# Kernel optimization log

Hardware: AMD Instinct MI355X
Metric: run time of the kernel (lower is better)

The kernel has to match this reference:

```python
import jax, jax.numpy as jnp
import numpy as np

N_PATCHES = 14
HIDDEN_D = 768
N_HEADS = 12
D_HEAD = HIDDEN_D // N_HEADS
SEQ = N_PATCHES ** 2 + 1  # 197
INPUT_D = 3 * 16 * 16  # c * patch_h * patch_w = 768
LN_EPS = 1e-5


def positional_embeddings(seq_len, d):
    # result[i, j] = sin(i / 10000**(j/d)) if j even else cos(i / 10000**((j-1)/d))
    i = jnp.arange(seq_len, dtype=jnp.float32)[:, None]
    j = jnp.arange(d, dtype=jnp.float32)[None, :]
    even = (jnp.arange(d) % 2 == 0)[None, :]
    denom_even = jnp.power(10000.0, j / d)
    denom_odd = jnp.power(10000.0, (j - 1.0) / d)
    return jnp.where(even, jnp.sin(i / denom_even), jnp.cos(i / denom_odd))


def setup_inputs() -> dict:
    key = jax.random.key(0)
    ks = jax.random.split(key, 12)
    s = 0.02
    return {
        "images": jax.random.normal(ks[0], (128, 3, 224, 224), dtype=jnp.float32),
        "W_map": jax.random.normal(ks[1], (HIDDEN_D, INPUT_D), dtype=jnp.float32) * s,
        "b_map": jax.random.normal(ks[2], (HIDDEN_D,), dtype=jnp.float32) * s,
        "class_token": jax.random.uniform(ks[3], (1, HIDDEN_D), dtype=jnp.float32),
        "ln_w": jnp.ones((SEQ, HIDDEN_D), dtype=jnp.float32),
        "ln_b": jnp.zeros((SEQ, HIDDEN_D), dtype=jnp.float32),
        "Wq": jax.random.normal(ks[4], (N_HEADS, D_HEAD, D_HEAD), dtype=jnp.float32) * s,
        "bq": jax.random.normal(ks[5], (N_HEADS, D_HEAD), dtype=jnp.float32) * s,
        "Wk": jax.random.normal(ks[6], (N_HEADS, D_HEAD, D_HEAD), dtype=jnp.float32) * s,
        "bk": jax.random.normal(ks[7], (N_HEADS, D_HEAD), dtype=jnp.float32) * s,
        "Wv": jax.random.normal(ks[8], (N_HEADS, D_HEAD, D_HEAD), dtype=jnp.float32) * s,
        "bv": jax.random.normal(ks[9], (N_HEADS, D_HEAD), dtype=jnp.float32) * s,
    }


def _forward(images, W_map, b_map, class_token, ln_w, ln_b, Wq, bq, Wk, bk, Wv, bv):
    n = images.shape[0]
    # naive patchify (faithful to source: a plain reshape)
    patches = images.reshape(n, N_PATCHES ** 2, INPUT_D)
    # linear mapper: x @ W.T + b
    tokens = jnp.einsum("npi,di->npd", patches, W_map) + b_map
    # prepend class token
    cls = jnp.broadcast_to(class_token[None], (n, 1, HIDDEN_D))
    tokens = jnp.concatenate([cls, tokens], axis=1)  # [n, SEQ, D]
    # positional embeddings
    tokens = tokens + positional_embeddings(SEQ, HIDDEN_D)[None]
    # LayerNorm over last two dims (SEQ, D) jointly
    mean = jnp.mean(tokens, axis=(-2, -1), keepdims=True)
    var = jnp.var(tokens, axis=(-2, -1), keepdims=True)
    x = (tokens - mean) / jnp.sqrt(var + LN_EPS) * ln_w + ln_b
    # multi-head self-attention (batched over samples and heads)
    xh = x.reshape(n, SEQ, N_HEADS, D_HEAD)  # head-sliced channels
    q = jnp.einsum("bshd,hed->bshe", xh, Wq) + bq[None, None]
    k = jnp.einsum("bshd,hed->bshe", xh, Wk) + bk[None, None]
    v = jnp.einsum("bshd,hed->bshe", xh, Wv) + bv[None, None]
    att = jax.nn.softmax(
        jnp.einsum("bshd,bthd->bhst", q, k) / jnp.sqrt(jnp.float32(D_HEAD)), axis=-1
    )
    msa = jnp.einsum("bhst,bthd->bshd", att, v).reshape(n, SEQ, HIDDEN_D)
    return tokens + msa


def reference(images, W_map, b_map, class_token, ln_w, ln_b, Wq, bq, Wk, bk, Wv, bv):
    return _forward(images, W_map, b_map, class_token, ln_w, ln_b, Wq, bq, Wk, bk, Wv, bv)
```

## Files before the change

kernel.cpp:

```cpp
#include <hip/hip_runtime.h>

typedef float fx4 __attribute__((ext_vector_type(4)));
typedef __bf16 bf16x8 __attribute__((ext_vector_type(8)));
typedef unsigned short ushort8 __attribute__((ext_vector_type(8)));
typedef unsigned int uint2v __attribute__((ext_vector_type(2)));
typedef unsigned int uint4v __attribute__((ext_vector_type(4)));

#define MFMA16(a, b, c) __builtin_amdgcn_mfma_f32_16x16x32_bf16((a), (b), (c), 0, 0, 0)

__device__ __forceinline__ unsigned short f2bf(float f) {
  unsigned int u = __float_as_uint(f);
  return (unsigned short)((u + 0x7FFFu + ((u >> 16) & 1u)) >> 16);
}

__device__ __forceinline__ ushort8 pack8(fx4 a, fx4 b) {
  ushort8 v;
  v[0] = f2bf(a[0]); v[1] = f2bf(a[1]); v[2] = f2bf(a[2]); v[3] = f2bf(a[3]);
  v[4] = f2bf(b[0]); v[5] = f2bf(b[1]); v[6] = f2bf(b[2]); v[7] = f2bf(b[3]);
  return v;
}

__device__ __forceinline__ uint2v pack2(fx4 v) {
  uint2v r;
  r[0] = (unsigned int)f2bf(v[0]) | ((unsigned int)f2bf(v[1]) << 16);
  r[1] = (unsigned int)f2bf(v[2]) | ((unsigned int)f2bf(v[3]) << 16);
  return r;
}

__device__ __forceinline__ bf16x8 xfrm(uint2v A, uint2v B, int quad, int src0, int src1) {
  uint4v pf;
#pragma unroll
  for (int d = 0; d < 2; d++) {
    int a0 = __shfl((int)A[d], src0, 64);
    int b0 = __shfl((int)B[d], src0, 64);
    pf[d] = (unsigned int)((quad < 2) ? a0 : b0);
    int a1 = __shfl((int)A[d], src1, 64);
    int b1 = __shfl((int)B[d], src1, 64);
    pf[2 + d] = (unsigned int)((quad < 2) ? a1 : b1);
  }
  return __builtin_bit_cast(bf16x8, pf);
}

__device__ __forceinline__ void gl2lds16(const unsigned short* g, void* lds_base) {
  __builtin_amdgcn_global_load_lds(
      (const __attribute__((address_space(1))) void*)(unsigned long long)(g),
      (__attribute__((address_space(3))) void*)(unsigned int)(unsigned long long)(lds_base),
      16, 0, 0);
}

__global__ void k_pe(float* __restrict__ pe, float* __restrict__ sums, float* __restrict__ sqs) {
  int idx = blockIdx.x * 256 + threadIdx.x;
  int s = idx / 768;
  int j = idx - s * 768;
  int jj = j & ~1;
  float ang = (float)s * expf((float)jj * (-9.210340371976184f / 768.0f));
  pe[idx] = (j & 1) ? cosf(ang) : sinf(ang);
  if (blockIdx.x == 0 && threadIdx.x < 128) {
    sums[threadIdx.x] = 0.f;
    sqs[threadIdx.x] = 0.f;
  }
}

__global__ void k_cvt(const float* __restrict__ img, const float* __restrict__ W,
                      unsigned short* __restrict__ imgbf, unsigned short* __restrict__ wbf) {
  size_t i = ((size_t)blockIdx.x * 256 + threadIdx.x) * 8;
  const float* src;
  unsigned short* dst;
  if (i < 19267584) { src = img + i; dst = imgbf + i; }
  else { size_t j = i - 19267584; src = W + j; dst = wbf + j; }
  const fx4* p = (const fx4*)src;
  *(ushort8*)dst = pack8(p[0], p[1]);
}

__global__ void k_wcvt(const float* __restrict__ Wq, const float* __restrict__ Wk,
                       const float* __restrict__ Wv, unsigned short* __restrict__ wqkv) {
  int i = (blockIdx.x * 256 + threadIdx.x) * 8;
  const float* src = (i < 49152) ? (Wq + i) : (i < 98304 ? Wk + (i - 49152) : Wv + (i - 98304));
  const fx4* p = (const fx4*)src;
  *(ushort8*)(wqkv + i) = pack8(p[0], p[1]);
}

__global__ __launch_bounds__(256) void k_tokens(
    const unsigned short* __restrict__ imgbf, const unsigned short* __restrict__ wbf,
    const float* __restrict__ bmap, const float* __restrict__ pe,
    float* __restrict__ out, float* __restrict__ sums, float* __restrict__ sqs) {
  __shared__ __align__(16) ushort8 Sf[16 * 64];
  if (blockIdx.x >= 196) return;
  const int tid = threadIdx.x;
  const int m0 = blockIdx.x * 128;
  const int n0 = blockIdx.y * 128;
  const int lane = tid & 63;
  const int w = tid >> 6;
  const int quad = lane >> 4, l16 = lane & 15;
  const int m_off = (w & 1) * 64, n_off = (w >> 1) * 64;

  fx4 acc[4][4];
#pragma unroll
  for (int i = 0; i < 4; i++)
#pragma unroll
    for (int j = 0; j < 4; j++) acc[i][j] = (fx4){0.f, 0.f, 0.f, 0.f};

  const unsigned short* pA = imgbf + (size_t)(m0 + w * 16 + l16) * 768 + quad * 8;
  const unsigned short* pB = wbf + (size_t)(n0 + w * 16 + l16) * 768 + quad * 8;
  void* lA0 = (void*)&Sf[(w) * 64];
  void* lA1 = (void*)&Sf[(4 + w) * 64];
  void* lB0 = (void*)&Sf[(8 + w) * 64];
  void* lB1 = (void*)&Sf[(12 + w) * 64];

  for (int k0 = 0; k0 < 768; k0 += 32) {
    __syncthreads();
    gl2lds16(pA + k0, lA0);
    gl2lds16(pA + 64 * 768 + k0, lA1);
    gl2lds16(pB + k0, lB0);
    gl2lds16(pB + 64 * 768 + k0, lB1);
    __syncthreads();
    bf16x8 a[4], b[4];
#pragma unroll
    for (int mt = 0; mt < 4; mt++)
      a[mt] = __builtin_bit_cast(bf16x8, Sf[((w & 1) * 4 + mt) * 64 + lane]);
#pragma unroll
    for (int nt = 0; nt < 4; nt++)
      b[nt] = __builtin_bit_cast(bf16x8, Sf[(8 + (w >> 1) * 4 + nt) * 64 + lane]);
#pragma unroll
    for (int mt = 0; mt < 4; mt++)
#pragma unroll
      for (int nt = 0; nt < 4; nt++) acc[mt][nt] = MFMA16(a[mt], b[nt], acc[mt][nt]);
  }

  float s0 = 0.f, q0 = 0.f, s1 = 0.f, q1 = 0.f;
  const int b0 = m0 / 196;
#pragma unroll
  for (int mt = 0; mt < 4; mt++) {
#pragma unroll
    for (int nt = 0; nt < 4; nt++) {
      const int col = n0 + n_off + nt * 16 + l16;
      const float bc = bmap[col];
#pragma unroll
      for (int r = 0; r < 4; r++) {
        const int gm = m0 + m_off + mt * 16 + quad * 4 + r;
        const int bb = gm / 196;
        const int ss = gm - bb * 196 + 1;
        float val = acc[mt][nt][r] + bc + pe[ss * 768 + col];
        out[((size_t)bb * 197 + ss) * 768 + col] = val;
        if (bb == b0) { s0 += val; q0 += val * val; }
        else          { s1 += val; q1 += val * val; }
      }
    }
  }
  for (int off = 32; off > 0; off >>= 1) {
    s0 += __shfl_down(s0, off); q0 += __shfl_down(q0, off);
    s1 += __shfl_down(s1, off); q1 += __shfl_down(q1, off);
  }
  if (lane == 0) {
    atomicAdd(&sums[b0], s0);
    atomicAdd(&sqs[b0], q0);
    if (b0 + 1 < 128) { atomicAdd(&sums[b0 + 1], s1); atomicAdd(&sqs[b0 + 1], q1); }
  }
}

__global__ __launch_bounds__(256) void k_cls(
    const float* __restrict__ ct, const float* __restrict__ pe,
    float* __restrict__ out, float* __restrict__ sums, float* __restrict__ sqs) {
  const int b = blockIdx.x, tid = threadIdx.x;
  float s = 0.f, q = 0.f;
#pragma unroll
  for (int it = 0; it < 3; it++) {
    int j = tid + it * 256;
    float v = ct[j] + pe[j];
    out[(size_t)b * 197 * 768 + j] = v;
    s += v; q += v * v;
  }
  for (int off = 32; off > 0; off >>= 1) { s += __shfl_down(s, off); q += __shfl_down(q, off); }
  __shared__ float rs[4], rq[4];
  int w = tid >> 6;
  if ((tid & 63) == 0) { rs[w] = s; rq[w] = q; }
  __syncthreads();
  if (tid == 0) {
    atomicAdd(&sums[b], rs[0] + rs[1] + rs[2] + rs[3]);
    atomicAdd(&sqs[b], rq[0] + rq[1] + rq[2] + rq[3]);
  }
}

__global__ void k_fin(const float* __restrict__ sums, const float* __restrict__ sqs,
                      float* __restrict__ mr) {
  int i = threadIdx.x;
  const float inv = 1.0f / 151296.0f;
  float m = sums[i] * inv;
  float v = sqs[i] * inv - m * m;
  mr[2 * i] = m;
  mr[2 * i + 1] = rsqrtf(v + 1e-5f);
}

__global__ __launch_bounds__(256, 2) void k_fused(
    const float* tok, const float* __restrict__ mr,
    const float* __restrict__ lnw, const float* __restrict__ lnb,
    const unsigned short* __restrict__ wqkv,
    const float* __restrict__ bq, const float* __restrict__ bk, const float* __restrict__ bv,
    float* out) {
  __shared__ __align__(16) ushort8 Kf[26 * 64];
  __shared__ __align__(16) ushort8 Vf[28 * 64];
  const int tid = threadIdx.x;
  const int bh = blockIdx.x;
  const int b = bh / 12;
  const int h = bh - b * 12;
  const int lane = tid & 63;
  const int w = tid >> 6;
  const int quad = lane >> 4;
  const int l16 = lane & 15;
  const int src0 = l16 + ((quad & 1) << 5);
  const int src1 = src0 + 16;
  const float mean = mr[2 * b], rstd = mr[2 * b + 1];
  const int hcol = h * 64;

  bf16x8 qfr[4][2];

  {
    bf16x8 wq[4][2], wk[4][2];
    fx4 bqv[4], bkv[4];
#pragma unroll
    for (int et = 0; et < 4; et++) {
      const int ro = (et * 16 + l16) * 64 + quad * 8;
#pragma unroll
      for (int kk = 0; kk < 2; kk++) {
        wq[et][kk] = *(const bf16x8*)(wqkv + h * 4096 + ro + kk * 32);
        wk[et][kk] = *(const bf16x8*)(wqkv + 49152 + h * 4096 + ro + kk * 32);
      }
      bqv[et] = *(const fx4*)(bq + hcol + et * 16 + quad * 4);
      bkv[et] = *(const fx4*)(bk + hcol + et * 16 + quad * 4);
    }
#pragma unroll
    for (int mi = 0; mi < 4; mi++) {
      const int mt = w + mi * 4;
      if (mt < 13) {
        int ss = mt * 16 + l16;
        ss = (ss < 197) ? ss : 196;
        bf16x8 xf[2];
#pragma unroll
        for (int kk = 0; kk < 2; kk++) {
          const int col = hcol + kk * 32 + quad * 8;
          const fx4* px = (const fx4*)(tok + (size_t)(b * 197 + ss) * 768 + col);
          const fx4* pw = (const fx4*)(lnw + (size_t)ss * 768 + col);
          const fx4* pb = (const fx4*)(lnb + (size_t)ss * 768 + col);
          fx4 y0 = (px[0] - mean) * rstd * pw[0] + pb[0];
          fx4 y1 = (px[1] - mean) * rstd * pw[1] + pb[1];
          xf[kk] = __builtin_bit_cast(bf16x8, pack8(y0, y1));
        }
        fx4 aq[4], ak[4];
#pragma unroll
        for (int et = 0; et < 4; et++) {
          aq[et] = (fx4){0.f, 0.f, 0.f, 0.f};
          ak[et] = (fx4){0.f, 0.f, 0.f, 0.f};
        }
#pragma unroll
        for (int kk = 0; kk < 2; kk++)
#pragma unroll
          for (int et = 0; et < 4; et++) {
            aq[et] = MFMA16(wq[et][kk], xf[kk], aq[et]);
            ak[et] = MFMA16(wk[et][kk], xf[kk], ak[et]);
          }
        uint2v qp[4], kp[4];
#pragma unroll
        for (int et = 0; et < 4; et++) {
          qp[et] = pack2(aq[et] + bqv[et]);
          kp[et] = pack2(ak[et] + bkv[et]);
        }
#pragma unroll
        for (int kk = 0; kk < 2; kk++) {
          qfr[mi][kk] = xfrm(qp[2 * kk], qp[2 * kk + 1], quad, src0, src1);
          bf16x8 kfrag = xfrm(kp[2 * kk], kp[2 * kk + 1], quad, src0, src1);
          Kf[(mt * 2 + kk) * 64 + lane] = __builtin_bit_cast(ushort8, kfrag);
        }
      }
    }
  }

  {
    bf16x8 wv[4][2];
    float bvs[4];
#pragma unroll
    for (int et = 0; et < 4; et++) {
      const int ro = (et * 16 + l16) * 64 + quad * 8;
#pragma unroll
      for (int kk = 0; kk < 2; kk++)
        wv[et][kk] = *(const bf16x8*)(wqkv + 98304 + h * 4096 + ro + kk * 32);
      bvs[et] = bv[hcol + et * 16 + l16];
    }
#pragma unroll
    for (int ji = 0; ji < 2; ji++) {
      const int jp = w + ji * 4;
      if (jp < 7) {
        fx4 av[2][4];
#pragma unroll
        for (int s2 = 0; s2 < 2; s2++)
#pragma unroll
          for (int et = 0; et < 4; et++) av[s2][et] = (fx4){0.f, 0.f, 0.f, 0.f};
#pragma unroll
        for (int s2 = 0; s2 < 2; s2++) {
          const int tt = 2 * jp + s2;
          if (tt < 13) {
            int ss = tt * 16 + l16;
            ss = (ss < 197) ? ss : 196;
            bf16x8 xf[2];
#pragma unroll
            for (int kk = 0; kk < 2; kk++) {
              const int col = hcol + kk * 32 + quad * 8;
              const fx4* px = (const fx4*)(tok + (size_t)(b * 197 + ss) * 768 + col);
              const fx4* pw = (const fx4*)(lnw + (size_t)ss * 768 + col);
              const fx4* pb = (const fx4*)(lnb + (size_t)ss * 768 + col);
              fx4 y0 = (px[0] - mean) * rstd * pw[0] + pb[0];
              fx4 y1 = (px[1] - mean) * rstd * pw[1] + pb[1];
              xf[kk] = __builtin_bit_cast(bf16x8, pack8(y0, y1));
            }
#pragma unroll
            for (int kk = 0; kk < 2; kk++)
#pragma unroll
              for (int et = 0; et < 4; et++)
                av[s2][et] = MFMA16(xf[kk], wv[et][kk], av[s2][et]);
          }
        }
#pragma unroll
        for (int et = 0; et < 4; et++) {
          fx4 bb = (fx4){bvs[et], bvs[et], bvs[et], bvs[et]};
          uint2v v0 = pack2(av[0][et] + bb);
          uint2v v1 = pack2(av[1][et] + bb);
          bf16x8 vfrag = xfrm(v0, v1, quad, src0, src1);
          Vf[(et * 7 + jp) * 64 + lane] = __builtin_bit_cast(ushort8, vfrag);
        }
      }
    }
  }
  __syncthreads();

#pragma unroll
  for (int mi = 0; mi < 4; mi++) {
    const int mt = w + mi * 4;
    if (mt < 13) {
      fx4 sacc[13];
#pragma unroll
      for (int nt = 0; nt < 13; nt++) sacc[nt] = (fx4){0.f, 0.f, 0.f, 0.f};
#pragma unroll
      for (int kk = 0; kk < 2; kk++) {
        bf16x8 qf = qfr[mi][kk];
#pragma unroll
        for (int nt = 0; nt < 13; nt++) {
          bf16x8 kf = __builtin_bit_cast(bf16x8, Kf[(nt * 2 + kk) * 64 + lane]);
          sacc[nt] = MFMA16(kf, qf, sacc[nt]);
        }
      }
      float sm = 0.f;
      uint2v pk[13];
#pragma unroll
      for (int nt = 0; nt < 13; nt++) {
        float p[4];
#pragma unroll
        for (int r = 0; r < 4; r++) {
          const bool valid = (nt < 12) | (quad * 4 + r < 5);
          p[r] = valid ? __expf(sacc[nt][r] * 0.125f) : 0.f;
          sm += p[r];
        }
        pk[nt][0] = (unsigned int)f2bf(p[0]) | ((unsigned int)f2bf(p[1]) << 16);
        pk[nt][1] = (unsigned int)f2bf(p[2]) | ((unsigned int)f2bf(p[3]) << 16);
      }
      sm += __shfl_xor(sm, 16);
      sm += __shfl_xor(sm, 32);
      const float inv = 1.0f / sm;

      fx4 oacc[4];
#pragma unroll
      for (int et = 0; et < 4; et++) oacc[et] = (fx4){0.f, 0.f, 0.f, 0.f};
#pragma unroll
      for (int kk = 0; kk < 7; kk++) {
        uint4v pf;
        if (kk < 6) {
          const int nA = 2 * kk, nB = 2 * kk + 1;
#pragma unroll
          for (int d = 0; d < 2; d++) {
            int a0 = __shfl((int)pk[nA][d], src0, 64);
            int b0 = __shfl((int)pk[nB][d], src0, 64);
            pf[d] = (unsigned int)((quad < 2) ? a0 : b0);
            int a1 = __shfl((int)pk[nA][d], src1, 64);
            int b1 = __shfl((int)pk[nB][d], src1, 64);
            pf[2 + d] = (unsigned int)((quad < 2) ? a1 : b1);
          }
        } else {
#pragma unroll
          for (int d = 0; d < 2; d++) {
            int a0 = __shfl((int)pk[12][d], src0, 64);
            pf[d] = (quad < 2) ? (unsigned int)a0 : 0u;
            int a1 = __shfl((int)pk[12][d], src1, 64);
            pf[2 + d] = (quad < 2) ? (unsigned int)a1 : 0u;
          }
        }
        bf16x8 pfrag = __builtin_bit_cast(bf16x8, pf);
#pragma unroll
        for (int et = 0; et < 4; et++) {
          bf16x8 vf = __builtin_bit_cast(bf16x8, Vf[(et * 7 + kk) * 64 + lane]);
          oacc[et] = MFMA16(vf, pfrag, oacc[et]);
        }
      }
      const int sg = mt * 16 + l16;
      if (sg < 197) {
        float* op = out + ((size_t)b * 197 + sg) * 768 + hcol + quad * 4;
#pragma unroll
        for (int et = 0; et < 4; et++) {
          fx4 cur = *(const fx4*)(op + et * 16);
          cur += oacc[et] * inv;
          *(fx4*)(op + et * 16) = cur;
        }
      }
    }
  }
}

extern "C" void kernel_launch(void* const* d_in, const int* in_sizes, int n_in,
                              void* d_out, int out_size, void* d_ws, size_t ws_size,
                              hipStream_t stream) {
  (void)in_sizes; (void)n_in; (void)out_size; (void)ws_size;
  const float* img  = (const float*)d_in[0];
  const float* Wmap = (const float*)d_in[1];
  const float* bmap = (const float*)d_in[2];
  const float* ct   = (const float*)d_in[3];
  const float* lnw  = (const float*)d_in[4];
  const float* lnb  = (const float*)d_in[5];
  const float* Wq   = (const float*)d_in[6];
  const float* bq   = (const float*)d_in[7];
  const float* Wk   = (const float*)d_in[8];
  const float* bk   = (const float*)d_in[9];
  const float* Wv   = (const float*)d_in[10];
  const float* bv   = (const float*)d_in[11];
  float* out = (float*)d_out;

  float* pe   = (float*)d_ws;
  float* sums = pe + 151296;
  float* sqs  = sums + 128;
  float* mr   = sqs + 128;
  unsigned short* wbf   = (unsigned short*)(mr + 256);
  unsigned short* imgbf = wbf + 589824;
  unsigned short* wqkv  = imgbf + (size_t)19267584;

  k_pe<<<591, 256, 0, stream>>>(pe, sums, sqs);
  k_cvt<<<9696, 256, 0, stream>>>(img, Wmap, imgbf, wbf);
  k_wcvt<<<72, 256, 0, stream>>>(Wq, Wk, Wv, wqkv);
  k_tokens<<<dim3(200, 6), 256, 0, stream>>>(imgbf, wbf, bmap, pe, out, sums, sqs);
  k_cls<<<128, 256, 0, stream>>>(ct, pe, out, sums, sqs);
  k_fin<<<1, 128, 0, stream>>>(sums, sqs, mr);
  k_fused<<<1536, 256, 0, stream>>>(out, mr, lnw, lnb, wqkv, bq, bk, bv, out);
}
```

Baseline: 355.5 us.

## Fuse QKV projection passes, shrink LDS, fold softmax scale into Q with exp2

The separate Q/K and V projection phases become a single pass, so each LayerNormed token tile is loaded and normalized once instead of twice. Q is pre-scaled by log2(e)/8 so softmax can use a raw exp2 builtin. The V LDS buffer is trimmed by storing only the valid half of the last tile, and launch bounds rise to 3 blocks per CU to improve occupancy. Keeping all three weight sets live together raises register pressure, which may conflict with the higher occupancy target and cause spills.

```diff
diff --git a/kernel.cpp b/kernel.cpp
--- a/kernel.cpp
+++ b/kernel.cpp
@@ -8,9 +8,14 @@
 
 #define MFMA16(a, b, c) __builtin_amdgcn_mfma_f32_16x16x32_bf16((a), (b), (c), 0, 0, 0)
 
+#if __has_builtin(__builtin_amdgcn_exp2f)
+#define EXP2(x) __builtin_amdgcn_exp2f(x)
+#else
+#define EXP2(x) exp2f(x)
+#endif
+
 __device__ __forceinline__ unsigned short f2bf(float f) {
-  unsigned int u = __float_as_uint(f);
-  return (unsigned short)((u + 0x7FFFu + ((u >> 16) & 1u)) >> 16);
+  return __builtin_bit_cast(unsigned short, (__bf16)f);
 }
 
 __device__ __forceinline__ ushort8 pack8(fx4 a, fx4 b) {
@@ -191,14 +196,15 @@
   mr[2 * i + 1] = rsqrtf(v + 1e-5f);
 }
 
-__global__ __launch_bounds__(256, 2) void k_fused(
+__global__ __launch_bounds__(256, 3) void k_fused(
     const float* tok, const float* __restrict__ mr,
     const float* __restrict__ lnw, const float* __restrict__ lnb,
     const unsigned short* __restrict__ wqkv,
     const float* __restrict__ bq, const float* __restrict__ bk, const float* __restrict__ bv,
     float* out) {
   __shared__ __align__(16) ushort8 Kf[26 * 64];
-  __shared__ __align__(16) ushort8 Vf[28 * 64];
+  __shared__ __align__(16) ushort8 Vf[24 * 64];
+  __shared__ __align__(16) ushort8 Vt[4 * 32];
   const int tid = threadIdx.x;
   const int bh = blockIdx.x;
   const int b = bh / 12;
@@ -214,133 +220,109 @@
 
   bf16x8 qfr[4][2];
 
-  {
-    bf16x8 wq[4][2], wk[4][2];
-    fx4 bqv[4], bkv[4];
-#pragma unroll
-    for (int et = 0; et < 4; et++) {
-      const int ro = (et * 16 + l16) * 64 + quad * 8;
-#pragma unroll
-      for (int kk = 0; kk < 2; kk++) {
-        wq[et][kk] = *(const bf16x8*)(wqkv + h * 4096 + ro + kk * 32);
-        wk[et][kk] = *(const bf16x8*)(wqkv + 49152 + h * 4096 + ro + kk * 32);
-      }
-      bqv[et] = *(const fx4*)(bq + hcol + et * 16 + quad * 4);
-      bkv[et] = *(const fx4*)(bk + hcol + et * 16 + quad * 4);
+  bf16x8 wq[4][2], wk[4][2], wv[4][2];
+#pragma unroll
+  for (int et = 0; et < 4; et++) {
+    const int ro = (et * 16 + l16) * 64 + quad * 8;
+#pragma unroll
+    for (int kk = 0; kk < 2; kk++) {
+      wq[et][kk] = *(const bf16x8*)(wqkv + hcol * 64 + ro + kk * 32);
+      wk[et][kk] = *(const bf16x8*)(wqkv + 49152 + hcol * 64 + ro + kk * 32);
+      wv[et][kk] = *(const bf16x8*)(wqkv + 98304 + hcol * 64 + ro + kk * 32);
     }
-#pragma unroll
-    for (int mi = 0; mi < 4; mi++) {
-      const int mt = w + mi * 4;
-      if (mt < 13) {
-        int ss = mt * 16 + l16;
-        ss = (ss < 197) ? ss : 196;
-        bf16x8 xf[2];
-#pragma unroll
-        for (int kk = 0; kk < 2; kk++) {
-          const int col = hcol + kk * 32 + quad * 8;
-          const fx4* px = (const fx4*)(tok + (size_t)(b * 197 + ss) * 768 + col);
-          const fx4* pw = (const fx4*)(lnw + (size_t)ss * 768 + col);
-          const fx4* pb = (const fx4*)(lnb + (size_t)ss * 768 + col);
-          fx4 y0 = (px[0] - mean) * rstd * pw[0] + pb[0];
-          fx4 y1 = (px[1] - mean) * rstd * pw[1] + pb[1];
-          xf[kk] = __builtin_bit_cast(bf16x8, pack8(y0, y1));
-        }
-        fx4 aq[4], ak[4];
-#pragma unroll
-        for (int et = 0; et < 4; et++) {
-          aq[et] = (fx4){0.f, 0.f, 0.f, 0.f};
-          ak[et] = (fx4){0.f, 0.f, 0.f, 0.f};
-        }
-#pragma unroll
-        for (int kk = 0; kk < 2; kk++)
+  }
+
+#pragma unroll
+  for (int pi = 0; pi < 2; pi++) {
+    const int jp = w + 4 * pi;
+    if (jp <= 6) {
+      bf16x8 xf[2][2];
+#pragma unroll
+      for (int s2 = 0; s2 < 2; s2++) {
+        const int tt = 2 * jp + s2;
+        if (tt < 13) {
+          int ss = tt * 16 + l16;
+          ss = (ss < 197) ? ss : 196;
+#pragma unroll
+          for (int kk = 0; kk < 2; kk++) {
+            const int col = hcol + kk * 32 + quad * 8;
+            const fx4* px = (const fx4*)(tok + (size_t)(b * 197 + ss) * 768 + col);
+            const fx4* pw = (const fx4*)(lnw + (size_t)ss * 768 + col);
+            const fx4* pb = (const fx4*)(lnb + (size_t)ss * 768 + col);
+            fx4 y0 = (px[0] - mean) * rstd * pw[0] + pb[0];
+            fx4 y1 = (px[1] - mean) * rstd * pw[1] + pb[1];
+            xf[s2][kk] = __builtin_bit_cast(bf16x8, pack8(y0, y1));
+          }
+          fx4 aq[4], ak[4];
 #pragma unroll
           for (int et = 0; et < 4; et++) {
-            aq[et] = MFMA16(wq[et][kk], xf[kk], aq[et]);
-            ak[et] = MFMA16(wk[et][kk], xf[kk], ak[et]);
-          }
-        uint2v qp[4], kp[4];
-#pragma unroll
-        for (int et = 0; et < 4; et++) {
-          qp[et] = pack2(aq[et] + bqv[et]);
-          kp[et] = pack2(ak[et] + bkv[et]);
-        }
-#pragma unroll
-        for (int kk = 0; kk < 2; kk++) {
-          qfr[mi][kk] = xfrm(qp[2 * kk], qp[2 * kk + 1], quad, src0, src1);
-          bf16x8 kfrag = xfrm(kp[2 * kk], kp[2 * kk + 1], quad, src0, src1);
-          Kf[(mt * 2 + kk) * 64 + lane] = __builtin_bit_cast(ushort8, kfrag);
-        }
+            aq[et] = (fx4){0.f, 0.f, 0.f, 0.f};
+            ak[et] = (fx4){0.f, 0.f, 0.f, 0.f};
+          }
+#pragma unroll
+          for (int kk = 0; kk < 2; kk++)
+#pragma unroll
+            for (int et = 0; et < 4; et++) {
+              aq[et] = MFMA16(wq[et][kk], xf[s2][kk], aq[et]);
+              ak[et] = MFMA16(wk[et][kk], xf[s2][kk], ak[et]);
+            }
+          uint2v qp[4], kp[4];
+#pragma unroll
+          for (int et = 0; et < 4; et++) {
+            fx4 bqv = *(const fx4*)(bq + hcol + et * 16 + quad * 4);
+            fx4 bkv = *(const fx4*)(bk + hcol + et * 16 + quad * 4);
+            qp[et] = pack2((aq[et] + bqv) * 0.18033688f);
+            kp[et] = pack2(ak[et] + bkv);
+          }
+          const int qi = pi * 2 + s2;
+#pragma unroll
+          for (int kk = 0; kk < 2; kk++) {
+            qfr[qi][kk] = xfrm(qp[2 * kk], qp[2 * kk + 1], quad, src0, src1);
+            bf16x8 kfrag = xfrm(kp[2 * kk], kp[2 * kk + 1], quad, src0, src1);
+            Kf[(tt * 2 + kk) * 64 + lane] = __builtin_bit_cast(ushort8, kfrag);
+          }
+        }
+      }
+      fx4 av[2][4];
+#pragma unroll
+      for (int s2 = 0; s2 < 2; s2++)
+#pragma unroll
+        for (int et = 0; et < 4; et++) av[s2][et] = (fx4){0.f, 0.f, 0.f, 0.f};
+#pragma unroll
+      for (int s2 = 0; s2 < 2; s2++) {
+        const int tt = 2 * jp + s2;
+        if (tt < 13) {
+#pragma unroll
+          for (int kk = 0; kk < 2; kk++)
+#pragma unroll
+            for (int et = 0; et < 4; et++)
+              av[s2][et] = MFMA16(xf[s2][kk], wv[et][kk], av[s2][et]);
+        }
+      }
+#pragma unroll
+      for (int et = 0; et < 4; et++) {
+        const float bvv = bv[hcol + et * 16 + l16];
+        fx4 bb4 = (fx4){bvv, bvv, bvv, bvv};
+        uint2v v0 = pack2(av[0][et] + bb4);
+        uint2v v1 = pack2(av[1][et] + bb4);
+        bf16x8 vfrag = xfrm(v0, v1, quad, src0, src1);
+        if (jp < 6) Vf[(et * 6 + jp) * 64 + lane] = __builtin_bit_cast(ushort8, vfrag);
+        else if (quad < 2) Vt[et * 32 + lane] = __builtin_bit_cast(ushort8, vfrag);
       }
     }
   }
-
-  {
-    bf16x8 wv[4][2];
-    float bvs[4];
-#pragma unroll
-    for (int et = 0; et < 4; et++) {
-      const int ro = (et * 16 + l16) * 64 + quad * 8;
-#pragma unroll
-      for (int kk = 0; kk < 2; kk++)
-        wv[et][kk] = *(const bf16x8*)(wqkv + 98304 + h * 4096 + ro + kk * 32);
-      bvs[et] = bv[hcol + et * 16 + l16];
-    }
-#pragma unroll
-    for (int ji = 0; ji < 2; ji++) {
-      const int jp = w + ji * 4;
-      if (jp < 7) {
-        fx4 av[2][4];
-#pragma unroll
-        for (int s2 = 0; s2 < 2; s2++)
-#pragma unroll
-          for (int et = 0; et < 4; et++) av[s2][et] = (fx4){0.f, 0.f, 0.f, 0.f};
-#pragma unroll
-        for (int s2 = 0; s2 < 2; s2++) {
-          const int tt = 2 * jp + s2;
-          if (tt < 13) {
-            int ss = tt * 16 + l16;
-            ss = (ss < 197) ? ss : 196;
-            bf16x8 xf[2];
-#pragma unroll
-            for (int kk = 0; kk < 2; kk++) {
-              const int col = hcol + kk * 32 + quad * 8;
-              const fx4* px = (const fx4*)(tok + (size_t)(b * 197 + ss) * 768 + col);
-              const fx4* pw = (const fx4*)(lnw + (size_t)ss * 768 + col);
-              const fx4* pb = (const fx4*)(lnb + (size_t)ss * 768 + col);
-              fx4 y0 = (px[0] - mean) * rstd * pw[0] + pb[0];
-              fx4 y1 = (px[1] - mean) * rstd * pw[1] + pb[1];
-              xf[kk] = __builtin_bit_cast(bf16x8, pack8(y0, y1));
-            }
-#pragma unroll
-            for (int kk = 0; kk < 2; kk++)
-#pragma unroll
-              for (int et = 0; et < 4; et++)
-                av[s2][et] = MFMA16(xf[kk], wv[et][kk], av[s2][et]);
-          }
-        }
-#pragma unroll
-        for (int et = 0; et < 4; et++) {
-          fx4 bb = (fx4){bvs[et], bvs[et], bvs[et], bvs[et]};
-          uint2v v0 = pack2(av[0][et] + bb);
-          uint2v v1 = pack2(av[1][et] + bb);
-          bf16x8 vfrag = xfrm(v0, v1, quad, src0, src1);
-          Vf[(et * 7 + jp) * 64 + lane] = __builtin_bit_cast(ushort8, vfrag);
-        }
-      }
-    }
-  }
   __syncthreads();
 
 #pragma unroll
-  for (int mi = 0; mi < 4; mi++) {
-    const int mt = w + mi * 4;
+  for (int qi = 0; qi < 4; qi++) {
+    const int mt = 2 * w + (qi >> 1) * 8 + (qi & 1);
     if (mt < 13) {
       fx4 sacc[13];
 #pragma unroll
       for (int nt = 0; nt < 13; nt++) sacc[nt] = (fx4){0.f, 0.f, 0.f, 0.f};
 #pragma unroll
       for (int kk = 0; kk < 2; kk++) {
-        bf16x8 qf = qfr[mi][kk];
+        bf16x8 qf = qfr[qi][kk];
 #pragma unroll
         for (int nt = 0; nt < 13; nt++) {
           bf16x8 kf = __builtin_bit_cast(bf16x8, Kf[(nt * 2 + kk) * 64 + lane]);
@@ -351,15 +333,14 @@
       uint2v pk[13];
 #pragma unroll
       for (int nt = 0; nt < 13; nt++) {
-        float p[4];
+        fx4 p;
 #pragma unroll
         for (int r = 0; r < 4; r++) {
           const bool valid = (nt < 12) | (quad * 4 + r < 5);
-          p[r] = valid ? __expf(sacc[nt][r] * 0.125f) : 0.f;
+          p[r] = valid ? EXP2(sacc[nt][r]) : 0.f;
           sm += p[r];
         }
-        pk[nt][0] = (unsigned int)f2bf(p[0]) | ((unsigned int)f2bf(p[1]) << 16);
-        pk[nt][1] = (unsigned int)f2bf(p[2]) | ((unsigned int)f2bf(p[3]) << 16);
+        pk[nt] = pack2(p);
       }
       sm += __shfl_xor(sm, 16);
       sm += __shfl_xor(sm, 32);
@@ -394,7 +375,15 @@
         bf16x8 pfrag = __builtin_bit_cast(bf16x8, pf);
 #pragma unroll
         for (int et = 0; et < 4; et++) {
-          bf16x8 vf = __builtin_bit_cast(bf16x8, Vf[(et * 7 + kk) * 64 + lane]);
+          bf16x8 vf;
+          if (kk < 6) {
+            vf = __builtin_bit_cast(bf16x8, Vf[(et * 6 + kk) * 64 + lane]);
+          } else if (quad < 2) {
+            vf = __builtin_bit_cast(bf16x8, Vt[et * 32 + lane]);
+          } else {
+            ushort8 z = {0, 0, 0, 0, 0, 0, 0, 0};
+            vf = __builtin_bit_cast(bf16x8, z);
+          }
           oacc[et] = MFMA16(vf, pfrag, oacc[et]);
         }
       }
```

New measurement: 358.3 us. Within noise of the previous version (+0.8%).
